# Kernel optimization log

Measured on AMD Instinct MI355X. Metric: run time of the kernel, lower is better.

The kernel has to match this reference:

```python
import jax, jax.numpy as jnp
import numpy as np

N, B, DIN, H, D, E = 20000, 2, 128, 4, 64, 320000
NEG_SLOPE = 0.2


def _leaky(x):
    return jnp.where(x >= 0, x, NEG_SLOPE * x)


def setup_inputs() -> dict:
    key = jax.random.key(0)
    k1, k2, k3, k4, k5, k6 = jax.random.split(key, 6)
    feat = jax.random.normal(k1, (N, B, DIN), dtype=jnp.float32)
    # fc weight, xavier-ish scale; stored as (Din, H*D) so projection is feat @ W
    W = jax.random.normal(k2, (DIN, H * D), dtype=jnp.float32) * (1.0 / np.sqrt(DIN))
    attn_l = jax.random.normal(k3, (H, D), dtype=jnp.float32) * 0.1
    attn_r = jax.random.normal(k4, (H, D), dtype=jnp.float32) * 0.1
    src = jax.random.randint(k5, (E,), 0, N, dtype=jnp.int32)
    dst = jax.random.randint(k6, (E,), 0, N, dtype=jnp.int32)
    return {"feat": feat, "W": W, "attn_l": attn_l, "attn_r": attn_r, "src": src, "dst": dst}


def reference(feat, W, attn_l, attn_r, src, dst):
    # feat: (N,B,Din) -> projected features (N,B,H,D)
    ft = (feat @ W).reshape(N, B, H, D)
    # per-node attention logits (N,B,H)
    el = jnp.einsum('nbhd,hd->nbh', ft, attn_l)
    er = jnp.einsum('nbhd,hd->nbh', ft, attn_r)
    # edge logits: u_add_v then LeakyReLU, shape (E,B,H)
    e = _leaky(el[src] + er[dst])
    # edge softmax normalized per destination node (numerically stable)
    emax = jax.ops.segment_max(e, dst, num_segments=N)
    emax = jnp.where(jnp.isfinite(emax), emax, 0.0)  # nodes with no in-edges
    ex = jnp.exp(e - emax[dst])
    denom = jax.ops.segment_sum(ex, dst, num_segments=N)
    a = ex / denom[dst]                               # (E,B,H); denom>0 for every edge's dst
    # u_mul_e messages and sum-aggregation by dst
    m = ft[src] * a[..., None]                        # (E,B,H,D)
    rst = jax.ops.segment_sum(m, dst, num_segments=N)  # (N,B,H,D)
    # module sets self.activation = leaky_relu unconditionally
    return _leaky(rst)
```

## Files before the change

kernel.cpp:

```cpp
#include <hip/hip_runtime.h>
#include <hip/hip_bf16.h>
#include <math.h>


typedef unsigned short ushort;
typedef __attribute__((ext_vector_type(8))) unsigned short ushort8;
typedef __attribute__((ext_vector_type(8))) short short8v;
typedef __attribute__((ext_vector_type(4))) float f32x4;

constexpr int DIN = 128;
constexpr int B   = 2;
constexpr int H   = 4;
constexpr int D   = 64;
constexpr int HD  = H * D;
constexpr int BHD = B * HD;
constexpr int NCOL = 272;
constexpr int PREP_ELEMS  = NCOL * DIN;
constexpr int PREP_BLOCKS = (PREP_ELEMS + 255) / 256;
constexpr int SXS = 72;

__device__ __forceinline__ float leaky(float x) { return x >= 0.f ? x : 0.2f * x; }

__device__ __forceinline__ ushort f2bf(float f) {
    return __builtin_bit_cast(ushort, __float2bfloat16(f));
}
__device__ __forceinline__ float bf2f(ushort v) {
    return __uint_as_float(((unsigned int)v) << 16);
}

__global__ __launch_bounds__(256) void hist_prep_kernel(
    const int* __restrict__ dst, int* __restrict__ deg, int E,
    const float* __restrict__ W, const float* __restrict__ attn_l,
    const float* __restrict__ attn_r, ushort* __restrict__ WT, int histBlocks)
{
    const int t = threadIdx.x;
    const int b = blockIdx.x;
    if (b < histBlocks) {
        int e4 = (b * 256 + t) * 4;
        if (e4 + 3 < E) {
            int4 dd = *(const int4*)(dst + e4);
            atomicAdd(&deg[dd.x], 1); atomicAdd(&deg[dd.y], 1);
            atomicAdd(&deg[dd.z], 1); atomicAdd(&deg[dd.w], 1);
        } else {
            for (int e = e4; e < E; ++e) atomicAdd(&deg[dst[e]], 1);
        }
        return;
    }
    int id = (b - histBlocks) * 256 + t;
    if (id >= PREP_ELEMS) return;
    int c = id >> 7, k = id & 127;
    float v;
    if (c < 256) {
        v = W[k * HD + c];
    } else if (c < 264) {
        int j = c - 256, h = j & 3;
        const float* av = (j < 4 ? attn_l : attn_r) + h * D;
        const float* wp = W + k * HD + h * D;
        float s = 0.f;
        for (int d = 0; d < D; ++d) s = fmaf(wp[d], av[d], s);
        v = s;
    } else {
        v = 0.f;
    }
    WT[c * DIN + k] = f2bf(v);
}

__device__ void scan_body(const int* __restrict__ deg, int* __restrict__ offs,
                          int* __restrict__ cursor, int n)
{
    __shared__ int wcarry[4];
    const int t = threadIdx.x;
    const int lane = t & 63;
    const int wid = t >> 6;
    int carry = 0;
    const int nstripes = (n + 1023) >> 10;
    for (int s = 0; s < nstripes; ++s) {
        const int base = (s << 10) + t * 4;
        int4 d = make_int4(0, 0, 0, 0);
        if (base + 3 < n) {
            d = *(const int4*)(deg + base);
        } else {
            if (base     < n) d.x = deg[base];
            if (base + 1 < n) d.y = deg[base + 1];
            if (base + 2 < n) d.z = deg[base + 2];
        }
        const int sum4 = (d.x + d.y) + (d.z + d.w);
        int inc = sum4;
#pragma unroll
        for (int o = 1; o < 64; o <<= 1) {
            int v = __shfl_up(inc, o, 64);
            if (lane >= o) inc += v;
        }
        if (lane == 63) wcarry[wid] = inc;
        __syncthreads();
        int wpre = carry;
#pragma unroll
        for (int k = 0; k < 4; ++k) if (k < wid) wpre += wcarry[k];
        const int e0 = wpre + inc - sum4;
        int4 ov;
        ov.x = e0; ov.y = e0 + d.x; ov.z = ov.y + d.y; ov.w = ov.z + d.z;
        if (base + 3 < n) {
            *(int4*)(offs + base) = ov;
            *(int4*)(cursor + base) = ov;
        } else {
            if (base     < n) { offs[base]     = ov.x; cursor[base]     = ov.x; }
            if (base + 1 < n) { offs[base + 1] = ov.y; cursor[base + 1] = ov.y; }
            if (base + 2 < n) { offs[base + 2] = ov.z; cursor[base + 2] = ov.z; }
        }
        carry += (wcarry[0] + wcarry[1]) + (wcarry[2] + wcarry[3]);
        __syncthreads();
    }
    if (t == 0) offs[n] = carry;
}

__global__ __launch_bounds__(256) void proj_scan_kernel(
    const float* __restrict__ feat, const ushort* __restrict__ WT,
    ushort* __restrict__ ftb, float* __restrict__ el, float* __restrict__ er,
    const int* __restrict__ deg, int* __restrict__ offs, int* __restrict__ cursor,
    int N, int nTiles)
{
    if ((int)blockIdx.x >= nTiles) {
        scan_body(deg, offs, cursor, N);
        return;
    }
    __shared__ ushort sxp[4][16][SXS];
    const int t = threadIdx.x;
    const int w = t >> 6;
    const int lane = t & 63;
    const int lr = lane & 15;
    const int lk = lane >> 4;

    short8v bfrag[4][4];
#pragma unroll
    for (int ct = 0; ct < 4; ++ct) {
        const int col = w * 64 + ct * 16 + lr;
#pragma unroll
        for (int ks = 0; ks < 4; ++ks)
            bfrag[ct][ks] = *(const short8v*)&WT[col * DIN + ks * 32 + lk * 8];
    }
    short8v efrag[4];
#pragma unroll
    for (int ks = 0; ks < 4; ++ks)
        efrag[ks] = *(const short8v*)&WT[(256 + lr) * DIN + ks * 32 + lk * 8];

    const int row0 = blockIdx.x * 64;
    ushort (* __restrict__ sw)[SXS] = sxp[w];
    const int rrow = lane >> 2;
    const int seg  = lane & 3;

#pragma unroll
    for (int rt = 0; rt < 4; ++rt) {
        const float* fp = feat + (size_t)(row0 + rt * 16 + lr) * DIN + lk * 8;
        short8v a[4];
#pragma unroll
        for (int ks = 0; ks < 4; ++ks) {
            f32x4 x0 = *(const f32x4*)(fp + ks * 32);
            f32x4 x1 = *(const f32x4*)(fp + ks * 32 + 4);
            short8v v;
            v[0] = (short)f2bf(x0[0]); v[1] = (short)f2bf(x0[1]);
            v[2] = (short)f2bf(x0[2]); v[3] = (short)f2bf(x0[3]);
            v[4] = (short)f2bf(x1[0]); v[5] = (short)f2bf(x1[1]);
            v[6] = (short)f2bf(x1[2]); v[7] = (short)f2bf(x1[3]);
            a[ks] = v;
        }

        f32x4 acc[4] = {{0.f,0.f,0.f,0.f},{0.f,0.f,0.f,0.f},{0.f,0.f,0.f,0.f},{0.f,0.f,0.f,0.f}};
#pragma unroll
        for (int ct = 0; ct < 4; ++ct)
#pragma unroll
            for (int ks = 0; ks < 4; ++ks)
                acc[ct] = __builtin_amdgcn_mfma_f32_16x16x32_bf16(a[ks], bfrag[ct][ks], acc[ct], 0, 0, 0);

#pragma unroll
        for (int ct = 0; ct < 4; ++ct)
#pragma unroll
            for (int r = 0; r < 4; ++r)
                sw[lk * 4 + r][ct * 16 + lr] = f2bf(acc[ct][r]);
        __builtin_amdgcn_wave_barrier();
        ushort8 o0 = *(const ushort8*)&sw[rrow][seg * 16];
        ushort8 o1 = *(const ushort8*)&sw[rrow][seg * 16 + 8];
        __builtin_amdgcn_wave_barrier();
        ushort* gp = ftb + (size_t)(row0 + rt * 16 + rrow) * HD + w * 64 + seg * 16;
        *(ushort8*)gp = o0;
        *(ushort8*)(gp + 8) = o1;

        if (rt == w) {
            f32x4 acce = {0.f, 0.f, 0.f, 0.f};
#pragma unroll
            for (int ks = 0; ks < 4; ++ks)
                acce = __builtin_amdgcn_mfma_f32_16x16x32_bf16(a[ks], efrag[ks], acce, 0, 0, 0);
#pragma unroll
            for (int r = 0; r < 4; ++r) {
                const int row = row0 + rt * 16 + lk * 4 + r;
                if (lr < 4)       el[row * 4 + lr]       = acce[r];
                else if (lr < 8)  er[row * 4 + (lr - 4)] = acce[r];
            }
        }
    }
}

__global__ __launch_bounds__(256) void scatter_kernel(
    const int* __restrict__ dst, const int* __restrict__ src,
    int* __restrict__ cursor, int* __restrict__ esrc, int E)
{
    int e4 = (blockIdx.x * 256 + threadIdx.x) * 4;
    if (e4 + 3 < E) {
        int4 dd = *(const int4*)(dst + e4);
        int4 ss = *(const int4*)(src + e4);
        int p0 = atomicAdd(&cursor[dd.x], 1); esrc[p0] = ss.x;
        int p1 = atomicAdd(&cursor[dd.y], 1); esrc[p1] = ss.y;
        int p2 = atomicAdd(&cursor[dd.z], 1); esrc[p2] = ss.z;
        int p3 = atomicAdd(&cursor[dd.w], 1); esrc[p3] = ss.w;
    } else {
        for (int e = e4; e < E; ++e) {
            int pos = atomicAdd(&cursor[dst[e]], 1);
            esrc[pos] = src[e];
        }
    }
}

__global__ __launch_bounds__(256) void agg_kernel(
    const ushort* __restrict__ ftb, const float* __restrict__ el,
    const float* __restrict__ er, const int* __restrict__ offs,
    const int* __restrict__ esrc, float* __restrict__ out, int N)
{
    const int t = threadIdx.x;
    const int n = blockIdx.x * 4 + (t >> 6);
    if (n >= N) return;
    const int lane = t & 63;
    const int bh = lane >> 3;
    const int beg = offs[n];
    const int end = offs[n + 1];

    const float erd = er[n * 8 + bh];
    const ushort8* __restrict__ ftv = (const ushort8*)ftb;

    float acc[8];
#pragma unroll
    for (int j = 0; j < 8; ++j) acc[j] = 0.f;
    float dsum = 0.f;

    int i = beg;
    for (; i + 7 < end; i += 8) {
        int s[8];
#pragma unroll
        for (int u = 0; u < 8; ++u) s[u] = esrc[i + u];
        float w[8];
#pragma unroll
        for (int u = 0; u < 8; ++u) w[u] = __expf(leaky(el[s[u] * 8 + bh] + erd));
        ushort8 v[8];
#pragma unroll
        for (int u = 0; u < 8; ++u) v[u] = ftv[s[u] * 64 + lane];
#pragma unroll
        for (int u = 0; u < 8; ++u) dsum += w[u];
#pragma unroll
        for (int j = 0; j < 8; ++j) {
            float a = acc[j];
#pragma unroll
            for (int u = 0; u < 8; ++u) a = fmaf(w[u], bf2f(v[u][j]), a);
            acc[j] = a;
        }
    }
    for (; i + 1 < end; i += 2) {
        int s0 = esrc[i], s1 = esrc[i + 1];
        float w0 = __expf(leaky(el[s0 * 8 + bh] + erd));
        float w1 = __expf(leaky(el[s1 * 8 + bh] + erd));
        ushort8 v0 = ftv[s0 * 64 + lane];
        ushort8 v1 = ftv[s1 * 64 + lane];
        dsum += w0 + w1;
#pragma unroll
        for (int j = 0; j < 8; ++j)
            acc[j] += w0 * bf2f(v0[j]) + w1 * bf2f(v1[j]);
    }
    if (i < end) {
        int s0 = esrc[i];
        float w0 = __expf(leaky(el[s0 * 8 + bh] + erd));
        ushort8 v0 = ftv[s0 * 64 + lane];
        dsum += w0;
#pragma unroll
        for (int j = 0; j < 8; ++j) acc[j] = fmaf(w0, bf2f(v0[j]), acc[j]);
    }

    const float sc = (end > beg) ? (1.f / dsum) : 0.f;
    float4 o0, o1;
    o0.x = leaky(acc[0] * sc); o0.y = leaky(acc[1] * sc);
    o0.z = leaky(acc[2] * sc); o0.w = leaky(acc[3] * sc);
    o1.x = leaky(acc[4] * sc); o1.y = leaky(acc[5] * sc);
    o1.z = leaky(acc[6] * sc); o1.w = leaky(acc[7] * sc);
    float* op = out + (size_t)n * BHD + lane * 8;
    *(float4*)op = o0;
    *(float4*)(op + 4) = o1;
}

extern "C" void kernel_launch(void* const* d_in, const int* in_sizes, int n_in,
                              void* d_out, int out_size, void* d_ws, size_t ws_size,
                              hipStream_t stream)
{
    const float* feat   = (const float*)d_in[0];
    const float* W      = (const float*)d_in[1];
    const float* attn_l = (const float*)d_in[2];
    const float* attn_r = (const float*)d_in[3];
    const int*   src    = (const int*)d_in[4];
    const int*   dst    = (const int*)d_in[5];
    float* out = (float*)d_out;

    const int N = in_sizes[0] / (B * DIN);
    const int E = in_sizes[4];
    const int R = N * B;
    const int nTiles = R / 64;
    const int histBlocks = (E / 4 + 255) / 256;
    const int edgeBlocks = histBlocks;

    auto align_up = [](size_t x) { return (x + 255) & ~(size_t)255; };
    size_t off = 0;
    char* base = (char*)d_ws;
    ushort* ftb = (ushort*)(base + off); off += align_up((size_t)R * HD * sizeof(ushort));
    float* el   = (float*)(base + off); off += align_up((size_t)R * H * sizeof(float));
    float* er   = (float*)(base + off); off += align_up((size_t)R * H * sizeof(float));
    ushort* WT  = (ushort*)(base + off); off += align_up((size_t)NCOL * DIN * sizeof(ushort));
    int* deg    = (int*)(base + off); off += align_up((size_t)N * sizeof(int));
    int* offs   = (int*)(base + off); off += align_up((size_t)(N + 1) * sizeof(int));
    int* cursor = (int*)(base + off); off += align_up((size_t)N * sizeof(int));
    int* esrc   = (int*)(base + off); off += align_up((size_t)E * sizeof(int));
    (void)ws_size; (void)n_in; (void)out_size;

    hipMemsetAsync(deg, 0, (size_t)N * sizeof(int), stream);

    hist_prep_kernel<<<histBlocks + PREP_BLOCKS, 256, 0, stream>>>(
        dst, deg, E, W, attn_l, attn_r, WT, histBlocks);
    proj_scan_kernel<<<nTiles + 1, 256, 0, stream>>>(
        feat, WT, ftb, el, er, deg, offs, cursor, N, nTiles);
    scatter_kernel<<<edgeBlocks, 256, 0, stream>>>(dst, src, cursor, esrc, E);
    agg_kernel<<<(N + 3) / 4, 256, 0, stream>>>(ftb, el, er, offs, esrc, out, N);
}
```

Baseline: 119.3 us.

## Precompute edge softmax weights in scatter and prefetch projection tiles

The scatter kernel now computes exp(leaky(el[src]+er[dst])) for all heads and batches per edge and stores it in CSR order. The aggregation kernel reads these weights instead of gathering el and recomputing exp. The projection kernel prefetches the next row tile's input while doing the MFMAs on the current one, and double-buffers the shared staging so one wave barrier can be dropped. The trade is an extra 32 bytes per edge written and read, plus random gathers in scatter, against less gather and exp work in aggregation.

```diff
diff --git a/kernel.cpp b/kernel.cpp
--- a/kernel.cpp
+++ b/kernel.cpp
@@ -123,7 +123,7 @@
         scan_body(deg, offs, cursor, N);
         return;
     }
-    __shared__ ushort sxp[4][16][SXS];
+    __shared__ ushort sxp[4][2][16][SXS];
     const int t = threadIdx.x;
     const int w = t >> 6;
     const int lane = t & 63;
@@ -144,14 +144,11 @@
         efrag[ks] = *(const short8v*)&WT[(256 + lr) * DIN + ks * 32 + lk * 8];
 
     const int row0 = blockIdx.x * 64;
-    ushort (* __restrict__ sw)[SXS] = sxp[w];
     const int rrow = lane >> 2;
     const int seg  = lane & 3;
 
-#pragma unroll
-    for (int rt = 0; rt < 4; ++rt) {
+    auto loadA = [&](int rt, short8v aout[4]) {
         const float* fp = feat + (size_t)(row0 + rt * 16 + lr) * DIN + lk * 8;
-        short8v a[4];
 #pragma unroll
         for (int ks = 0; ks < 4; ++ks) {
             f32x4 x0 = *(const f32x4*)(fp + ks * 32);
@@ -161,16 +158,25 @@
             v[2] = (short)f2bf(x0[2]); v[3] = (short)f2bf(x0[3]);
             v[4] = (short)f2bf(x1[0]); v[5] = (short)f2bf(x1[1]);
             v[6] = (short)f2bf(x1[2]); v[7] = (short)f2bf(x1[3]);
-            a[ks] = v;
-        }
+            aout[ks] = v;
+        }
+    };
+
+    short8v aP[4], aN[4];
+    loadA(0, aP);
+
+#pragma unroll
+    for (int rt = 0; rt < 4; ++rt) {
+        if (rt < 3) loadA(rt + 1, aN);
 
         f32x4 acc[4] = {{0.f,0.f,0.f,0.f},{0.f,0.f,0.f,0.f},{0.f,0.f,0.f,0.f},{0.f,0.f,0.f,0.f}};
 #pragma unroll
         for (int ct = 0; ct < 4; ++ct)
 #pragma unroll
             for (int ks = 0; ks < 4; ++ks)
-                acc[ct] = __builtin_amdgcn_mfma_f32_16x16x32_bf16(a[ks], bfrag[ct][ks], acc[ct], 0, 0, 0);
-
+                acc[ct] = __builtin_amdgcn_mfma_f32_16x16x32_bf16(aP[ks], bfrag[ct][ks], acc[ct], 0, 0, 0);
+
+        ushort (* __restrict__ sw)[SXS] = sxp[w][rt & 1];
 #pragma unroll
         for (int ct = 0; ct < 4; ++ct)
 #pragma unroll
@@ -179,7 +185,6 @@
         __builtin_amdgcn_wave_barrier();
         ushort8 o0 = *(const ushort8*)&sw[rrow][seg * 16];
         ushort8 o1 = *(const ushort8*)&sw[rrow][seg * 16 + 8];
-        __builtin_amdgcn_wave_barrier();
         ushort* gp = ftb + (size_t)(row0 + rt * 16 + rrow) * HD + w * 64 + seg * 16;
         *(ushort8*)gp = o0;
         *(ushort8*)(gp + 8) = o1;
@@ -188,7 +193,7 @@
             f32x4 acce = {0.f, 0.f, 0.f, 0.f};
 #pragma unroll
             for (int ks = 0; ks < 4; ++ks)
-                acce = __builtin_amdgcn_mfma_f32_16x16x32_bf16(a[ks], efrag[ks], acce, 0, 0, 0);
+                acce = __builtin_amdgcn_mfma_f32_16x16x32_bf16(aP[ks], efrag[ks], acce, 0, 0, 0);
 #pragma unroll
             for (int r = 0; r < 4; ++r) {
                 const int row = row0 + rt * 16 + lk * 4 + r;
@@ -196,33 +201,50 @@
                 else if (lr < 8)  er[row * 4 + (lr - 4)] = acce[r];
             }
         }
+
+#pragma unroll
+        for (int ks = 0; ks < 4; ++ks) aP[ks] = aN[ks];
     }
 }
 
 __global__ __launch_bounds__(256) void scatter_kernel(
     const int* __restrict__ dst, const int* __restrict__ src,
-    int* __restrict__ cursor, int* __restrict__ esrc, int E)
-{
+    const float* __restrict__ el, const float* __restrict__ er,
+    int* __restrict__ cursor, int* __restrict__ esrc, float* __restrict__ ew, int E)
+{
+    auto doEdge = [&](int s, int d) {
+        int pos = atomicAdd(&cursor[d], 1);
+        esrc[pos] = s;
+        const float* elp = el + (size_t)s * 8;
+        const float* erp = er + (size_t)d * 8;
+        f32x4 a0 = *(const f32x4*)elp;
+        f32x4 a1 = *(const f32x4*)(elp + 4);
+        f32x4 b0 = *(const f32x4*)erp;
+        f32x4 b1 = *(const f32x4*)(erp + 4);
+        f32x4 w0, w1;
+#pragma unroll
+        for (int j = 0; j < 4; ++j) w0[j] = __expf(leaky(a0[j] + b0[j]));
+#pragma unroll
+        for (int j = 0; j < 4; ++j) w1[j] = __expf(leaky(a1[j] + b1[j]));
+        float* wp = ew + (size_t)pos * 8;
+        *(f32x4*)wp = w0;
+        *(f32x4*)(wp + 4) = w1;
+    };
     int e4 = (blockIdx.x * 256 + threadIdx.x) * 4;
     if (e4 + 3 < E) {
         int4 dd = *(const int4*)(dst + e4);
         int4 ss = *(const int4*)(src + e4);
-        int p0 = atomicAdd(&cursor[dd.x], 1); esrc[p0] = ss.x;
-        int p1 = atomicAdd(&cursor[dd.y], 1); esrc[p1] = ss.y;
-        int p2 = atomicAdd(&cursor[dd.z], 1); esrc[p2] = ss.z;
-        int p3 = atomicAdd(&cursor[dd.w], 1); esrc[p3] = ss.w;
+        doEdge(ss.x, dd.x); doEdge(ss.y, dd.y);
+        doEdge(ss.z, dd.z); doEdge(ss.w, dd.w);
     } else {
-        for (int e = e4; e < E; ++e) {
-            int pos = atomicAdd(&cursor[dst[e]], 1);
-            esrc[pos] = src[e];
-        }
+        for (int e = e4; e < E; ++e) doEdge(src[e], dst[e]);
     }
 }
 
 __global__ __launch_bounds__(256) void agg_kernel(
-    const ushort* __restrict__ ftb, const float* __restrict__ el,
-    const float* __restrict__ er, const int* __restrict__ offs,
-    const int* __restrict__ esrc, float* __restrict__ out, int N)
+    const ushort* __restrict__ ftb, const float* __restrict__ ew,
+    const int* __restrict__ offs, const int* __restrict__ esrc,
+    float* __restrict__ out, int N)
 {
     const int t = threadIdx.x;
     const int n = blockIdx.x * 4 + (t >> 6);
@@ -232,7 +254,6 @@
     const int beg = offs[n];
     const int end = offs[n + 1];
 
-    const float erd = er[n * 8 + bh];
     const ushort8* __restrict__ ftv = (const ushort8*)ftb;
 
     float acc[8];
@@ -247,10 +268,10 @@
         for (int u = 0; u < 8; ++u) s[u] = esrc[i + u];
         float w[8];
 #pragma unroll
-        for (int u = 0; u < 8; ++u) w[u] = __expf(leaky(el[s[u] * 8 + bh] + erd));
+        for (int u = 0; u < 8; ++u) w[u] = ew[(size_t)(i + u) * 8 + bh];
         ushort8 v[8];
 #pragma unroll
-        for (int u = 0; u < 8; ++u) v[u] = ftv[s[u] * 64 + lane];
+        for (int u = 0; u < 8; ++u) v[u] = ftv[(size_t)s[u] * 64 + lane];
 #pragma unroll
         for (int u = 0; u < 8; ++u) dsum += w[u];
 #pragma unroll
@@ -263,10 +284,10 @@
     }
     for (; i + 1 < end; i += 2) {
         int s0 = esrc[i], s1 = esrc[i + 1];
-        float w0 = __expf(leaky(el[s0 * 8 + bh] + erd));
-        float w1 = __expf(leaky(el[s1 * 8 + bh] + erd));
-        ushort8 v0 = ftv[s0 * 64 + lane];
-        ushort8 v1 = ftv[s1 * 64 + lane];
+        float w0 = ew[(size_t)i * 8 + bh];
+        float w1 = ew[(size_t)(i + 1) * 8 + bh];
+        ushort8 v0 = ftv[(size_t)s0 * 64 + lane];
+        ushort8 v1 = ftv[(size_t)s1 * 64 + lane];
         dsum += w0 + w1;
 #pragma unroll
         for (int j = 0; j < 8; ++j)
@@ -274,8 +295,8 @@
     }
     if (i < end) {
         int s0 = esrc[i];
-        float w0 = __expf(leaky(el[s0 * 8 + bh] + erd));
-        ushort8 v0 = ftv[s0 * 64 + lane];
+        float w0 = ew[(size_t)i * 8 + bh];
+        ushort8 v0 = ftv[(size_t)s0 * 64 + lane];
         dsum += w0;
 #pragma unroll
         for (int j = 0; j < 8; ++j) acc[j] = fmaf(w0, bf2f(v0[j]), acc[j]);
@@ -322,6 +343,7 @@
     int* offs   = (int*)(base + off); off += align_up((size_t)(N + 1) * sizeof(int));
     int* cursor = (int*)(base + off); off += align_up((size_t)N * sizeof(int));
     int* esrc   = (int*)(base + off); off += align_up((size_t)E * sizeof(int));
+    float* ew   = (float*)(base + off); off += align_up((size_t)E * 8 * sizeof(float));
     (void)ws_size; (void)n_in; (void)out_size;
 
     hipMemsetAsync(deg, 0, (size_t)N * sizeof(int), stream);
@@ -330,6 +352,6 @@
         dst, deg, E, W, attn_l, attn_r, WT, histBlocks);
     proj_scan_kernel<<<nTiles + 1, 256, 0, stream>>>(
         feat, WT, ftb, el, er, deg, offs, cursor, N, nTiles);
-    scatter_kernel<<<edgeBlocks, 256, 0, stream>>>(dst, src, cursor, esrc, E);
-    agg_kernel<<<(N + 3) / 4, 256, 0, stream>>>(ftb, el, er, offs, esrc, out, N);
-}
+    scatter_kernel<<<edgeBlocks, 256, 0, stream>>>(dst, src, el, er, cursor, esrc, ew, E);
+    agg_kernel<<<(N + 3) / 4, 256, 0, stream>>>(ftb, ew, offs, esrc, out, N);
+}
```

After: 128.3 us. +7.6%, slower.

## Persist projection blocks over two tiles with prefetched A fragments and double-buffered LDS

Applied to the files above, without the earlier changes.

The projection kernel now launches about half as many blocks, and each block loops over several 64-row tiles, so the B-fragment register loads are amortised. The next row tile's feat load and bf16 conversion are issued before the current tile's MFMAs, and the LDS staging buffer is double-buffered so the second wave barrier can be dropped. In the aggregation kernel the feature-row gathers are moved ahead of the exp weight computation and use unsigned indexing, to get the long-latency loads in flight earlier. The cost is higher register pressure from the prefetch buffers and fewer blocks in flight for the projection.

```diff
diff --git a/kernel.cpp b/kernel.cpp
--- a/kernel.cpp
+++ b/kernel.cpp
@@ -119,11 +119,12 @@
     const int* __restrict__ deg, int* __restrict__ offs, int* __restrict__ cursor,
     int N, int nTiles)
 {
-    if ((int)blockIdx.x >= nTiles) {
+    const int PB = gridDim.x - 1;
+    if ((int)blockIdx.x >= PB) {
         scan_body(deg, offs, cursor, N);
         return;
     }
-    __shared__ ushort sxp[4][16][SXS];
+    __shared__ ushort sxp[4][2][16][SXS];
     const int t = threadIdx.x;
     const int w = t >> 6;
     const int lane = t & 63;
@@ -143,58 +144,69 @@
     for (int ks = 0; ks < 4; ++ks)
         efrag[ks] = *(const short8v*)&WT[(256 + lr) * DIN + ks * 32 + lk * 8];
 
-    const int row0 = blockIdx.x * 64;
-    ushort (* __restrict__ sw)[SXS] = sxp[w];
     const int rrow = lane >> 2;
     const int seg  = lane & 3;
 
-#pragma unroll
-    for (int rt = 0; rt < 4; ++rt) {
-        const float* fp = feat + (size_t)(row0 + rt * 16 + lr) * DIN + lk * 8;
-        short8v a[4];
-#pragma unroll
-        for (int ks = 0; ks < 4; ++ks) {
-            f32x4 x0 = *(const f32x4*)(fp + ks * 32);
-            f32x4 x1 = *(const f32x4*)(fp + ks * 32 + 4);
-            short8v v;
-            v[0] = (short)f2bf(x0[0]); v[1] = (short)f2bf(x0[1]);
-            v[2] = (short)f2bf(x0[2]); v[3] = (short)f2bf(x0[3]);
-            v[4] = (short)f2bf(x1[0]); v[5] = (short)f2bf(x1[1]);
-            v[6] = (short)f2bf(x1[2]); v[7] = (short)f2bf(x1[3]);
-            a[ks] = v;
-        }
-
-        f32x4 acc[4] = {{0.f,0.f,0.f,0.f},{0.f,0.f,0.f,0.f},{0.f,0.f,0.f,0.f},{0.f,0.f,0.f,0.f}};
-#pragma unroll
-        for (int ct = 0; ct < 4; ++ct)
-#pragma unroll
-            for (int ks = 0; ks < 4; ++ks)
-                acc[ct] = __builtin_amdgcn_mfma_f32_16x16x32_bf16(a[ks], bfrag[ct][ks], acc[ct], 0, 0, 0);
-
-#pragma unroll
-        for (int ct = 0; ct < 4; ++ct)
-#pragma unroll
-            for (int r = 0; r < 4; ++r)
-                sw[lk * 4 + r][ct * 16 + lr] = f2bf(acc[ct][r]);
-        __builtin_amdgcn_wave_barrier();
-        ushort8 o0 = *(const ushort8*)&sw[rrow][seg * 16];
-        ushort8 o1 = *(const ushort8*)&sw[rrow][seg * 16 + 8];
-        __builtin_amdgcn_wave_barrier();
-        ushort* gp = ftb + (size_t)(row0 + rt * 16 + rrow) * HD + w * 64 + seg * 16;
-        *(ushort8*)gp = o0;
-        *(ushort8*)(gp + 8) = o1;
-
-        if (rt == w) {
-            f32x4 acce = {0.f, 0.f, 0.f, 0.f};
-#pragma unroll
-            for (int ks = 0; ks < 4; ++ks)
-                acce = __builtin_amdgcn_mfma_f32_16x16x32_bf16(a[ks], efrag[ks], acce, 0, 0, 0);
-#pragma unroll
-            for (int r = 0; r < 4; ++r) {
-                const int row = row0 + rt * 16 + lk * 4 + r;
-                if (lr < 4)       el[row * 4 + lr]       = acce[r];
-                else if (lr < 8)  er[row * 4 + (lr - 4)] = acce[r];
+    for (int tile = blockIdx.x; tile < nTiles; tile += PB) {
+        const int row0 = tile * 64;
+
+        auto loadA = [&](int rt, short8v aout[4]) {
+            const float* fp = feat + (size_t)(row0 + rt * 16 + lr) * DIN + lk * 8;
+#pragma unroll
+            for (int ks = 0; ks < 4; ++ks) {
+                f32x4 x0 = *(const f32x4*)(fp + ks * 32);
+                f32x4 x1 = *(const f32x4*)(fp + ks * 32 + 4);
+                short8v v;
+                v[0] = (short)f2bf(x0[0]); v[1] = (short)f2bf(x0[1]);
+                v[2] = (short)f2bf(x0[2]); v[3] = (short)f2bf(x0[3]);
+                v[4] = (short)f2bf(x1[0]); v[5] = (short)f2bf(x1[1]);
+                v[6] = (short)f2bf(x1[2]); v[7] = (short)f2bf(x1[3]);
+                aout[ks] = v;
             }
+        };
+
+        short8v aP[4], aN[4];
+        loadA(0, aP);
+
+#pragma unroll
+        for (int rt = 0; rt < 4; ++rt) {
+            if (rt < 3) loadA(rt + 1, aN);
+
+            f32x4 acc[4] = {{0.f,0.f,0.f,0.f},{0.f,0.f,0.f,0.f},{0.f,0.f,0.f,0.f},{0.f,0.f,0.f,0.f}};
+#pragma unroll
+            for (int ct = 0; ct < 4; ++ct)
+#pragma unroll
+                for (int ks = 0; ks < 4; ++ks)
+                    acc[ct] = __builtin_amdgcn_mfma_f32_16x16x32_bf16(aP[ks], bfrag[ct][ks], acc[ct], 0, 0, 0);
+
+            ushort (* __restrict__ sw)[SXS] = sxp[w][rt & 1];
+#pragma unroll
+            for (int ct = 0; ct < 4; ++ct)
+#pragma unroll
+                for (int r = 0; r < 4; ++r)
+                    sw[lk * 4 + r][ct * 16 + lr] = f2bf(acc[ct][r]);
+            __builtin_amdgcn_wave_barrier();
+            ushort8 o0 = *(const ushort8*)&sw[rrow][seg * 16];
+            ushort8 o1 = *(const ushort8*)&sw[rrow][seg * 16 + 8];
+            ushort* gp = ftb + (size_t)(row0 + rt * 16 + rrow) * HD + w * 64 + seg * 16;
+            *(ushort8*)gp = o0;
+            *(ushort8*)(gp + 8) = o1;
+
+            if (rt == w) {
+                f32x4 acce = {0.f, 0.f, 0.f, 0.f};
+#pragma unroll
+                for (int ks = 0; ks < 4; ++ks)
+                    acce = __builtin_amdgcn_mfma_f32_16x16x32_bf16(aP[ks], efrag[ks], acce, 0, 0, 0);
+#pragma unroll
+                for (int r = 0; r < 4; ++r) {
+                    const int row = row0 + rt * 16 + lk * 4 + r;
+                    if (lr < 4)       el[row * 4 + lr]       = acce[r];
+                    else if (lr < 8)  er[row * 4 + (lr - 4)] = acce[r];
+                }
+            }
+
+#pragma unroll
+            for (int ks = 0; ks < 4; ++ks) aP[ks] = aN[ks];
         }
     }
 }
@@ -245,12 +257,12 @@
         int s[8];
 #pragma unroll
         for (int u = 0; u < 8; ++u) s[u] = esrc[i + u];
+        ushort8 v[8];
+#pragma unroll
+        for (int u = 0; u < 8; ++u) v[u] = ftv[(unsigned)s[u] * 64 + lane];
         float w[8];
 #pragma unroll
         for (int u = 0; u < 8; ++u) w[u] = __expf(leaky(el[s[u] * 8 + bh] + erd));
-        ushort8 v[8];
-#pragma unroll
-        for (int u = 0; u < 8; ++u) v[u] = ftv[s[u] * 64 + lane];
 #pragma unroll
         for (int u = 0; u < 8; ++u) dsum += w[u];
 #pragma unroll
@@ -263,10 +275,10 @@
     }
     for (; i + 1 < end; i += 2) {
         int s0 = esrc[i], s1 = esrc[i + 1];
+        ushort8 v0 = ftv[(unsigned)s0 * 64 + lane];
+        ushort8 v1 = ftv[(unsigned)s1 * 64 + lane];
         float w0 = __expf(leaky(el[s0 * 8 + bh] + erd));
         float w1 = __expf(leaky(el[s1 * 8 + bh] + erd));
-        ushort8 v0 = ftv[s0 * 64 + lane];
-        ushort8 v1 = ftv[s1 * 64 + lane];
         dsum += w0 + w1;
 #pragma unroll
         for (int j = 0; j < 8; ++j)
@@ -274,8 +286,8 @@
     }
     if (i < end) {
         int s0 = esrc[i];
+        ushort8 v0 = ftv[(unsigned)s0 * 64 + lane];
         float w0 = __expf(leaky(el[s0 * 8 + bh] + erd));
-        ushort8 v0 = ftv[s0 * 64 + lane];
         dsum += w0;
 #pragma unroll
         for (int j = 0; j < 8; ++j) acc[j] = fmaf(w0, bf2f(v0[j]), acc[j]);
@@ -308,6 +320,7 @@
     const int E = in_sizes[4];
     const int R = N * B;
     const int nTiles = R / 64;
+    const int projBlocks = (nTiles + 1) / 2;
     const int histBlocks = (E / 4 + 255) / 256;
     const int edgeBlocks = histBlocks;
 
@@ -328,7 +341,7 @@
 
     hist_prep_kernel<<<histBlocks + PREP_BLOCKS, 256, 0, stream>>>(
         dst, deg, E, W, attn_l, attn_r, WT, histBlocks);
-    proj_scan_kernel<<<nTiles + 1, 256, 0, stream>>>(
+    proj_scan_kernel<<<projBlocks + 1, 256, 0, stream>>>(
         feat, WT, ftb, el, er, deg, offs, cursor, N, nTiles);
     scatter_kernel<<<edgeBlocks, 256, 0, stream>>>(dst, src, cursor, esrc, E);
     agg_kernel<<<(N + 3) / 4, 256, 0, stream>>>(ftb, el, er, offs, esrc, out, N);
```

Result: no change. 120.9 us (+1.3%).
